# Optimization experiments

Hardware: AMD Instinct MI355X
Metric: run time of the kernel (lower is better)

## Reference

```python
import jax, jax.numpy as jnp
import numpy as np

B, F, G, L, C = 32768, 512, 16, 64, 1000  # batch, feature_dim, n_groups, labels/group, num_classes


def setup_inputs() -> dict:
    key = jax.random.key(0)
    k1, k2, k3, k4, k5 = jax.random.split(key, 5)
    features = jax.random.normal(k1, (B, F), dtype=jnp.float32)
    group_probs = jax.random.uniform(k2, (B, G), dtype=jnp.float32)
    # stacked per-group Linear heads: W[g] is the (L, F) weight of head g, b[g] its bias
    W = jax.random.normal(k3, (G, L, F), dtype=jnp.float32) / np.sqrt(F).astype(np.float32)
    b = jax.random.normal(k4, (G, L), dtype=jnp.float32) * 0.01
    # group_to_labels: label_ids[g, j] = shared class id that head g's j-th output maps to
    label_ids = jax.random.randint(k5, (G, L), 0, C, dtype=jnp.int32)
    return {"features": features, "group_probs": group_probs, "W": W, "b": b,
            "label_ids": label_ids}


def reference(features, group_probs, W, b, label_ids):
    # all per-group linear heads as one batched GEMM: [B,G,L]
    group_logits = jnp.einsum('bf,glf->bgl', features, W) + b
    # weight each group's logits by its group probability
    weighted = group_probs[:, :, None] * group_logits          # [B, G, L]
    # scatter-add into the shared logit tensor (duplicate class ids accumulate)
    flat_idx = label_ids.reshape(-1)                            # [G*L]
    logits = jnp.zeros((features.shape[0], C), dtype=features.dtype)
    logits = logits.at[:, flat_idx].add(weighted.reshape(features.shape[0], -1))
    return logits
```

## Files before the change

kernel.cpp:

```cpp
#include <hip/hip_runtime.h>
#include <stdint.h>

#define B_SZ   32768
#define F_SZ   512
#define G_SZ   16
#define L_SZ   64
#define N_COLS 1024
#define C_SZ   1000
#define M_TILE 64
#define A_STRIDE 520
#define W_STRIDE 1042
#define SMEM_BYTES 66688

typedef __attribute__((ext_vector_type(8))) short short8;
typedef __attribute__((ext_vector_type(4))) float floatx4;

__device__ __forceinline__ unsigned short f2bf(float f) {
    unsigned int x = __float_as_uint(f);
    x += 0x7fffu + ((x >> 16) & 1u);
    return (unsigned short)(x >> 16);
}

__device__ __forceinline__ void barrier_lgkm() {
    __builtin_amdgcn_sched_barrier(0);
    asm volatile("s_waitcnt lgkmcnt(0)" ::: "memory");
    __builtin_amdgcn_s_barrier();
    __builtin_amdgcn_sched_barrier(0);
}

__global__ __launch_bounds__(1024) void build_csr_kernel(const int* __restrict__ label_ids,
                                                         const float* __restrict__ bias,
                                                         int* __restrict__ off,
                                                         int* __restrict__ list,
                                                         float* __restrict__ bias_p,
                                                         unsigned char* __restrict__ g_perm) {
    __shared__ int cnt[1024];
    __shared__ int cur[1024];
    const int t = threadIdx.x;
    cnt[t] = 0;
    __syncthreads();
    const int lbl = label_ids[t];
    atomicAdd(&cnt[lbl], 1);
    __syncthreads();
    int v = cnt[t];
    #pragma unroll
    for (int d = 1; d < 1024; d <<= 1) {
        int u = (t >= d) ? cnt[t - d] : 0;
        __syncthreads();
        v += u;
        cnt[t] = v;
        __syncthreads();
    }
    int ex = (t == 0) ? 0 : cnt[t - 1];
    cur[t] = ex;
    if (t <= C_SZ) off[t] = (t == 0) ? 0 : cnt[t - 1];
    __syncthreads();
    int pos = atomicAdd(&cur[lbl], 1);
    list[pos]   = t;
    bias_p[pos] = bias[t];
    g_perm[pos] = (unsigned char)(t >> 6);
}

__global__ __launch_bounds__(256) void convert_w_kernel(const float* __restrict__ W,
                                                        const int* __restrict__ list,
                                                        unsigned short* __restrict__ Wb) {
    int idx = blockIdx.x * 256 + threadIdx.x;
    int row = idx >> 7;
    int c4  = idx & 127;
    int src = list[row];
    const float4* W4 = (const float4*)W;
    float4 v = W4[src * 128 + c4];
    ushort4 u = make_ushort4(f2bf(v.x), f2bf(v.y), f2bf(v.z), f2bf(v.w));
    ((ushort4*)Wb)[idx] = u;
}

__global__ __launch_bounds__(1024, 4) void mhc_main_kernel(
        const float* __restrict__ feat,
        const float* __restrict__ gp,
        const unsigned short* __restrict__ Wb,
        const float* __restrict__ bias_p,
        const int* __restrict__ off,
        const unsigned char* __restrict__ g_perm,
        float* __restrict__ out)
{
    __shared__ __align__(16) char smem[SMEM_BYTES];
    __shared__ float gp_s[M_TILE * G_SZ];
    __shared__ float bias_s[N_COLS];
    __shared__ unsigned char g_s[N_COLS];

    unsigned short* As = (unsigned short*)smem;
    float* WL = (float*)smem;

    const int t    = threadIdx.x;
    const int wave = t >> 6;
    const int lane = t & 63;
    const int m16  = lane & 15;
    const int quad = lane >> 4;
    const int r0   = blockIdx.x * M_TILE;

    gp_s[t]   = gp[r0 * G_SZ + t];
    bias_s[t] = bias_p[t];
    g_s[t]    = g_perm[t];

    int e0 = 0, e1 = 0;
    if (t < C_SZ) { e0 = off[t]; e1 = off[t + 1]; }

    {
        const float4* f4 = (const float4*)(feat + (size_t)r0 * F_SZ);
        #pragma unroll
        for (int i = 0; i < 8; ++i) {
            int idx = t + i * 1024;
            int row = idx >> 7;
            int c4  = idx & 127;
            float4 v = f4[idx];
            ushort4 u = make_ushort4(f2bf(v.x), f2bf(v.y), f2bf(v.z), f2bf(v.w));
            *(ushort4*)(As + row * A_STRIDE + c4 * 4) = u;
        }
    }
    barrier_lgkm();

    const floatx4 zero = {0.f, 0.f, 0.f, 0.f};
    floatx4 acc[4][4];
    #pragma unroll
    for (int i = 0; i < 4; ++i)
        #pragma unroll
        for (int j = 0; j < 4; ++j) acc[i][j] = zero;

    const unsigned short* aBase = As + m16 * A_STRIDE + quad * 8;
    const unsigned short* bBase = Wb + (size_t)(wave * 64 + m16) * F_SZ + quad * 8;

    #pragma unroll 4
    for (int kt = 0; kt < 16; ++kt) {
        short8 a[4];
        #pragma unroll
        for (int rt = 0; rt < 4; ++rt)
            a[rt] = *(const short8*)(aBase + rt * 16 * A_STRIDE + kt * 32);
        #pragma unroll
        for (int ct = 0; ct < 4; ++ct) {
            short8 b = *(const short8*)(bBase + ct * 16 * F_SZ + kt * 32);
            #pragma unroll
            for (int rt = 0; rt < 4; ++rt)
                acc[rt][ct] = __builtin_amdgcn_mfma_f32_16x16x32_bf16(a[rt], b, acc[rt][ct], 0, 0, 0);
        }
    }

    #pragma unroll
    for (int p = 0; p < 4; ++p) {
        barrier_lgkm();
        #pragma unroll
        for (int ct = 0; ct < 4; ++ct) {
            int col = wave * 64 + ct * 16 + m16;
            int g   = g_s[col];
            float bi = bias_s[col];
            #pragma unroll
            for (int r = 0; r < 4; ++r) {
                int rl = quad * 4 + r;
                float v = gp_s[(p * 16 + rl) * G_SZ + g] * (acc[p][ct][r] + bi);
                WL[rl * W_STRIDE + col] = v;
            }
        }
        barrier_lgkm();
        if (t < C_SZ) {
            #pragma unroll
            for (int h = 0; h < 4; ++h) {
                float s0 = 0.f, s1 = 0.f, s2 = 0.f, s3 = 0.f;
                for (int j = e0; j < e1; ++j) {
                    s0 += WL[(h * 4 + 0) * W_STRIDE + j];
                    s1 += WL[(h * 4 + 1) * W_STRIDE + j];
                    s2 += WL[(h * 4 + 2) * W_STRIDE + j];
                    s3 += WL[(h * 4 + 3) * W_STRIDE + j];
                }
                size_t rowg = (size_t)(r0 + p * 16 + h * 4);
                out[(rowg + 0) * C_SZ + t] = s0;
                out[(rowg + 1) * C_SZ + t] = s1;
                out[(rowg + 2) * C_SZ + t] = s2;
                out[(rowg + 3) * C_SZ + t] = s3;
            }
        }
    }
}

extern "C" void kernel_launch(void* const* d_in, const int* in_sizes, int n_in,
                              void* d_out, int out_size, void* d_ws, size_t ws_size,
                              hipStream_t stream) {
    const float* feat  = (const float*)d_in[0];
    const float* gp    = (const float*)d_in[1];
    const float* W     = (const float*)d_in[2];
    const float* bias  = (const float*)d_in[3];
    const int* labels  = (const int*)d_in[4];
    float* out = (float*)d_out;

    unsigned short* Wb = (unsigned short*)d_ws;
    char* base = (char*)d_ws + (1 << 20);
    int* off             = (int*)base;
    int* list            = (int*)(base + 4096);
    float* bias_p        = (float*)(base + 8192);
    unsigned char* g_prm = (unsigned char*)(base + 12288);

    build_csr_kernel<<<1, 1024, 0, stream>>>(labels, bias, off, list, bias_p, g_prm);
    convert_w_kernel<<<(N_COLS * F_SZ / 4) / 256, 256, 0, stream>>>(W, list, Wb);
    mhc_main_kernel<<<B_SZ / M_TILE, 1024, 0, stream>>>(feat, gp, Wb, bias_p, off, g_prm, out);
}
```

Before: 258.0 us.

## Replace CSR gather reduction with LDS atomic scatter-add into class buffer

Drops the CSR build kernel and the permuted weight layout, and scatters each weighted logit with an LDS float atomicAdd into a 16x1024 per-tile output buffer indexed by class id. The buffer is then written to global memory and zeroed. This removes one kernel launch and the serial per-class gather loop with its uneven lengths. In exchange it adds LDS atomic contention on duplicate class ids, an extra zeroing pass and barriers, and makes the order of float accumulation nondeterministic.

```diff
diff --git a/kernel.cpp b/kernel.cpp
--- a/kernel.cpp
+++ b/kernel.cpp
@@ -9,8 +9,8 @@
 #define C_SZ   1000
 #define M_TILE 64
 #define A_STRIDE 520
-#define W_STRIDE 1042
-#define SMEM_BYTES 66688
+#define OUT_STRIDE 1024
+#define SMEM_WORDS 16640
 
 typedef __attribute__((ext_vector_type(8))) short short8;
 typedef __attribute__((ext_vector_type(4))) float floatx4;
@@ -28,48 +28,11 @@
     __builtin_amdgcn_sched_barrier(0);
 }
 
-__global__ __launch_bounds__(1024) void build_csr_kernel(const int* __restrict__ label_ids,
-                                                         const float* __restrict__ bias,
-                                                         int* __restrict__ off,
-                                                         int* __restrict__ list,
-                                                         float* __restrict__ bias_p,
-                                                         unsigned char* __restrict__ g_perm) {
-    __shared__ int cnt[1024];
-    __shared__ int cur[1024];
-    const int t = threadIdx.x;
-    cnt[t] = 0;
-    __syncthreads();
-    const int lbl = label_ids[t];
-    atomicAdd(&cnt[lbl], 1);
-    __syncthreads();
-    int v = cnt[t];
-    #pragma unroll
-    for (int d = 1; d < 1024; d <<= 1) {
-        int u = (t >= d) ? cnt[t - d] : 0;
-        __syncthreads();
-        v += u;
-        cnt[t] = v;
-        __syncthreads();
-    }
-    int ex = (t == 0) ? 0 : cnt[t - 1];
-    cur[t] = ex;
-    if (t <= C_SZ) off[t] = (t == 0) ? 0 : cnt[t - 1];
-    __syncthreads();
-    int pos = atomicAdd(&cur[lbl], 1);
-    list[pos]   = t;
-    bias_p[pos] = bias[t];
-    g_perm[pos] = (unsigned char)(t >> 6);
-}
-
 __global__ __launch_bounds__(256) void convert_w_kernel(const float* __restrict__ W,
-                                                        const int* __restrict__ list,
                                                         unsigned short* __restrict__ Wb) {
     int idx = blockIdx.x * 256 + threadIdx.x;
-    int row = idx >> 7;
-    int c4  = idx & 127;
-    int src = list[row];
     const float4* W4 = (const float4*)W;
-    float4 v = W4[src * 128 + c4];
+    float4 v = W4[idx];
     ushort4 u = make_ushort4(f2bf(v.x), f2bf(v.y), f2bf(v.z), f2bf(v.w));
     ((ushort4*)Wb)[idx] = u;
 }
@@ -78,18 +41,17 @@
         const float* __restrict__ feat,
         const float* __restrict__ gp,
         const unsigned short* __restrict__ Wb,
-        const float* __restrict__ bias_p,
-        const int* __restrict__ off,
-        const unsigned char* __restrict__ g_perm,
+        const float* __restrict__ bias,
+        const int* __restrict__ labels,
         float* __restrict__ out)
 {
-    __shared__ __align__(16) char smem[SMEM_BYTES];
+    __shared__ __align__(16) float smem[SMEM_WORDS];
     __shared__ float gp_s[M_TILE * G_SZ];
     __shared__ float bias_s[N_COLS];
-    __shared__ unsigned char g_s[N_COLS];
+    __shared__ unsigned short cls_s[N_COLS];
 
     unsigned short* As = (unsigned short*)smem;
-    float* WL = (float*)smem;
+    float* OL = smem;
 
     const int t    = threadIdx.x;
     const int wave = t >> 6;
@@ -99,11 +61,8 @@
     const int r0   = blockIdx.x * M_TILE;
 
     gp_s[t]   = gp[r0 * G_SZ + t];
-    bias_s[t] = bias_p[t];
-    g_s[t]    = g_perm[t];
-
-    int e0 = 0, e1 = 0;
-    if (t < C_SZ) { e0 = off[t]; e1 = off[t + 1]; }
+    bias_s[t] = bias[t];
+    cls_s[t]  = (unsigned short)labels[t];
 
     {
         const float4* f4 = (const float4*)(feat + (size_t)r0 * F_SZ);
@@ -144,39 +103,38 @@
         }
     }
 
+    barrier_lgkm();
+    {
+        #pragma unroll
+        for (int i = 0; i < 4; ++i)
+            *(floatx4*)(OL + i * 4096 + t * 4) = zero;
+    }
+    barrier_lgkm();
+
     #pragma unroll
     for (int p = 0; p < 4; ++p) {
-        barrier_lgkm();
         #pragma unroll
         for (int ct = 0; ct < 4; ++ct) {
             int col = wave * 64 + ct * 16 + m16;
-            int g   = g_s[col];
+            int cls = cls_s[col];
             float bi = bias_s[col];
             #pragma unroll
             for (int r = 0; r < 4; ++r) {
                 int rl = quad * 4 + r;
-                float v = gp_s[(p * 16 + rl) * G_SZ + g] * (acc[p][ct][r] + bi);
-                WL[rl * W_STRIDE + col] = v;
+                float v = gp_s[(p * 16 + rl) * G_SZ + wave] * (acc[p][ct][r] + bi);
+                atomicAdd(&OL[rl * OUT_STRIDE + cls], v);
             }
         }
         barrier_lgkm();
         if (t < C_SZ) {
             #pragma unroll
-            for (int h = 0; h < 4; ++h) {
-                float s0 = 0.f, s1 = 0.f, s2 = 0.f, s3 = 0.f;
-                for (int j = e0; j < e1; ++j) {
-                    s0 += WL[(h * 4 + 0) * W_STRIDE + j];
-                    s1 += WL[(h * 4 + 1) * W_STRIDE + j];
-                    s2 += WL[(h * 4 + 2) * W_STRIDE + j];
-                    s3 += WL[(h * 4 + 3) * W_STRIDE + j];
-                }
-                size_t rowg = (size_t)(r0 + p * 16 + h * 4);
-                out[(rowg + 0) * C_SZ + t] = s0;
-                out[(rowg + 1) * C_SZ + t] = s1;
-                out[(rowg + 2) * C_SZ + t] = s2;
-                out[(rowg + 3) * C_SZ + t] = s3;
+            for (int h = 0; h < 16; ++h) {
+                float v = OL[h * OUT_STRIDE + t];
+                OL[h * OUT_STRIDE + t] = 0.f;
+                out[(size_t)(r0 + p * 16 + h) * C_SZ + t] = v;
             }
         }
+        barrier_lgkm();
     }
 }
 
@@ -191,13 +149,7 @@
     float* out = (float*)d_out;
 
     unsigned short* Wb = (unsigned short*)d_ws;
-    char* base = (char*)d_ws + (1 << 20);
-    int* off             = (int*)base;
-    int* list            = (int*)(base + 4096);
-    float* bias_p        = (float*)(base + 8192);
-    unsigned char* g_prm = (unsigned char*)(base + 12288);
 
-    build_csr_kernel<<<1, 1024, 0, stream>>>(labels, bias, off, list, bias_p, g_prm);
-    convert_w_kernel<<<(N_COLS * F_SZ / 4) / 256, 256, 0, stream>>>(W, list, Wb);
-    mhc_main_kernel<<<B_SZ / M_TILE, 1024, 0, stream>>>(feat, gp, Wb, bias_p, off, g_prm, out);
+    convert_w_kernel<<<(N_COLS * F_SZ / 4) / 256, 256, 0, stream>>>(W, Wb);
+    mhc_main_kernel<<<B_SZ / M_TILE, 1024, 0, stream>>>(feat, gp, Wb, bias, labels, out);
 }
```

After: 405.1 us. 57.0% more time.

## Transpose weighted-logit staging and sort classes by fan-in for balanced gather

Applied to the files above, without the earlier changes.

The epilogue now stores the weighted logits transposed (column-major with stride 20) using vector stores, so each class's gather reads four floatx4 values per source column instead of sixteen scalar strided loads. Classes are also sorted by the number of contributing columns in the CSR build, so threads in a wave have similar loop trip counts and divergence drops. Output stores become scattered by class id rather than contiguous per thread index, which can hurt write coalescing. Shared memory grows to 81920 bytes, which may lower occupancy.

```diff
diff --git a/kernel.cpp b/kernel.cpp
--- a/kernel.cpp
+++ b/kernel.cpp
@@ -9,8 +9,8 @@
 #define C_SZ   1000
 #define M_TILE 64
 #define A_STRIDE 520
-#define W_STRIDE 1042
-#define SMEM_BYTES 66688
+#define WT_STRIDE 20
+#define SMEM_BYTES 81920
 
 typedef __attribute__((ext_vector_type(8))) short short8;
 typedef __attribute__((ext_vector_type(4))) float floatx4;
@@ -30,14 +30,19 @@
 
 __global__ __launch_bounds__(1024) void build_csr_kernel(const int* __restrict__ label_ids,
                                                          const float* __restrict__ bias,
-                                                         int* __restrict__ off,
                                                          int* __restrict__ list,
                                                          float* __restrict__ bias_p,
-                                                         unsigned char* __restrict__ g_perm) {
+                                                         unsigned char* __restrict__ g_perm,
+                                                         int* __restrict__ srt_cls,
+                                                         int* __restrict__ srt_off,
+                                                         int* __restrict__ srt_len) {
     __shared__ int cnt[1024];
     __shared__ int cur[1024];
+    __shared__ int hist2[64];
+    __shared__ int start2[64];
     const int t = threadIdx.x;
     cnt[t] = 0;
+    if (t < 64) hist2[t] = 0;
     __syncthreads();
     const int lbl = label_ids[t];
     atomicAdd(&cnt[lbl], 1);
@@ -51,14 +56,28 @@
         cnt[t] = v;
         __syncthreads();
     }
-    int ex = (t == 0) ? 0 : cnt[t - 1];
+    int ex  = (t == 0) ? 0 : cnt[t - 1];
+    int len = v - ex;
     cur[t] = ex;
-    if (t <= C_SZ) off[t] = (t == 0) ? 0 : cnt[t - 1];
     __syncthreads();
     int pos = atomicAdd(&cur[lbl], 1);
     list[pos]   = t;
     bias_p[pos] = bias[t];
     g_perm[pos] = (unsigned char)(t >> 6);
+    int lc = (len < 63) ? len : 63;
+    if (t < C_SZ) atomicAdd(&hist2[lc], 1);
+    __syncthreads();
+    if (t == 0) {
+        int run = 0;
+        for (int k = 63; k >= 0; --k) { start2[k] = run; run += hist2[k]; }
+    }
+    __syncthreads();
+    if (t < C_SZ) {
+        int rk = atomicAdd(&start2[lc], 1);
+        srt_cls[rk] = t;
+        srt_off[rk] = ex;
+        srt_len[rk] = len;
+    }
 }
 
 __global__ __launch_bounds__(256) void convert_w_kernel(const float* __restrict__ W,
@@ -79,8 +98,10 @@
         const float* __restrict__ gp,
         const unsigned short* __restrict__ Wb,
         const float* __restrict__ bias_p,
-        const int* __restrict__ off,
         const unsigned char* __restrict__ g_perm,
+        const int* __restrict__ srt_cls,
+        const int* __restrict__ srt_off,
+        const int* __restrict__ srt_len,
         float* __restrict__ out)
 {
     __shared__ __align__(16) char smem[SMEM_BYTES];
@@ -89,7 +110,7 @@
     __shared__ unsigned char g_s[N_COLS];
 
     unsigned short* As = (unsigned short*)smem;
-    float* WL = (float*)smem;
+    float* WT = (float*)smem;
 
     const int t    = threadIdx.x;
     const int wave = t >> 6;
@@ -102,8 +123,8 @@
     bias_s[t] = bias_p[t];
     g_s[t]    = g_perm[t];
 
-    int e0 = 0, e1 = 0;
-    if (t < C_SZ) { e0 = off[t]; e1 = off[t + 1]; }
+    int cls = 0, e0 = 0, len = 0;
+    if (t < C_SZ) { cls = srt_cls[t]; e0 = srt_off[t]; len = srt_len[t]; }
 
     {
         const float4* f4 = (const float4*)(feat + (size_t)r0 * F_SZ);
@@ -152,29 +173,31 @@
             int col = wave * 64 + ct * 16 + m16;
             int g   = g_s[col];
             float bi = bias_s[col];
+            floatx4 w;
             #pragma unroll
             for (int r = 0; r < 4; ++r) {
                 int rl = quad * 4 + r;
-                float v = gp_s[(p * 16 + rl) * G_SZ + g] * (acc[p][ct][r] + bi);
-                WL[rl * W_STRIDE + col] = v;
+                w[r] = gp_s[(p * 16 + rl) * G_SZ + g] * (acc[p][ct][r] + bi);
             }
+            *(floatx4*)(WT + col * WT_STRIDE + quad * 4) = w;
         }
         barrier_lgkm();
         if (t < C_SZ) {
+            floatx4 s0 = zero, s1 = zero, s2 = zero, s3 = zero;
+            for (int j = e0; j < e0 + len; ++j) {
+                const float* cb = WT + j * WT_STRIDE;
+                s0 += *(const floatx4*)(cb + 0);
+                s1 += *(const floatx4*)(cb + 4);
+                s2 += *(const floatx4*)(cb + 8);
+                s3 += *(const floatx4*)(cb + 12);
+            }
+            size_t rb = (size_t)(r0 + p * 16) * C_SZ + cls;
             #pragma unroll
-            for (int h = 0; h < 4; ++h) {
-                float s0 = 0.f, s1 = 0.f, s2 = 0.f, s3 = 0.f;
-                for (int j = e0; j < e1; ++j) {
-                    s0 += WL[(h * 4 + 0) * W_STRIDE + j];
-                    s1 += WL[(h * 4 + 1) * W_STRIDE + j];
-                    s2 += WL[(h * 4 + 2) * W_STRIDE + j];
-                    s3 += WL[(h * 4 + 3) * W_STRIDE + j];
-                }
-                size_t rowg = (size_t)(r0 + p * 16 + h * 4);
-                out[(rowg + 0) * C_SZ + t] = s0;
-                out[(rowg + 1) * C_SZ + t] = s1;
-                out[(rowg + 2) * C_SZ + t] = s2;
-                out[(rowg + 3) * C_SZ + t] = s3;
+            for (int r = 0; r < 4; ++r) {
+                out[rb + (size_t)(r +  0) * C_SZ] = s0[r];
+                out[rb + (size_t)(r +  4) * C_SZ] = s1[r];
+                out[rb + (size_t)(r +  8) * C_SZ] = s2[r];
+                out[rb + (size_t)(r + 12) * C_SZ] = s3[r];
             }
         }
     }
@@ -192,12 +215,16 @@
 
     unsigned short* Wb = (unsigned short*)d_ws;
     char* base = (char*)d_ws + (1 << 20);
-    int* off             = (int*)base;
-    int* list            = (int*)(base + 4096);
-    float* bias_p        = (float*)(base + 8192);
-    unsigned char* g_prm = (unsigned char*)(base + 12288);
-
-    build_csr_kernel<<<1, 1024, 0, stream>>>(labels, bias, off, list, bias_p, g_prm);
+    int* list            = (int*)(base);
+    float* bias_p        = (float*)(base + 4096);
+    unsigned char* g_prm = (unsigned char*)(base + 8192);
+    int* srt_cls         = (int*)(base + 12288);
+    int* srt_off         = (int*)(base + 16384);
+    int* srt_len         = (int*)(base + 20480);
+
+    build_csr_kernel<<<1, 1024, 0, stream>>>(labels, bias, list, bias_p, g_prm,
+                                             srt_cls, srt_off, srt_len);
     convert_w_kernel<<<(N_COLS * F_SZ / 4) / 256, 256, 0, stream>>>(W, list, Wb);
-    mhc_main_kernel<<<B_SZ / M_TILE, 1024, 0, stream>>>(feat, gp, Wb, bias_p, off, g_prm, out);
-}
+    mhc_main_kernel<<<B_SZ / M_TILE, 1024, 0, stream>>>(feat, gp, Wb, bias_p, g_prm,
+                                                        srt_cls, srt_off, srt_len, out);
+}
```

New measurement: 278.5 us. 1.08x slower.
